# Kernel optimization log

Measured on AMD Instinct MI355X. Metric: run time of the kernel, lower is better.

Reference implementation:

```python
import jax, jax.numpy as jnp
import numpy as np

LOG_2PI = 1.8378770664093453  # log(2*pi)

B, N_FEAT = 4096, 1024
R, K, D = 64, 32, 16  # n_regions, n_batch (distributions per region), region size


def setup_inputs() -> dict:
    key = jax.random.key(0)
    k1, k2, k3, k4 = jax.random.split(key, 4)
    x = jax.random.normal(k1, (B, N_FEAT), dtype=jnp.float32)
    # Regions: partition-like index sets over the feature space (equal size D).
    regions = jax.random.randint(k2, (R, D), 0, N_FEAT, dtype=jnp.int64)
    # Per-region diag-Gaussian params (means ~ N(0, 0.1), scales near 1.0).
    means = 0.1 * jax.random.normal(k3, (R, K, D), dtype=jnp.float32)
    scales = 0.9 + 0.2 * jax.random.uniform(k4, (R, K, D), dtype=jnp.float32)
    return {"x": x, "regions": regions, "means": means, "scales": scales}


def reference(x, regions, means, scales):
    # Gather per-region features in one shot: [B, R, D]
    xg = x[:, regions]
    # Diag-Gaussian log-prob, broadcast over the K distributions per region.
    # z: [B, R, K, D]
    z = (xg[:, :, None, :] - means[None]) / scales[None]
    log_det = jnp.sum(jnp.log(scales), axis=-1)  # [R, K]
    ll = -0.5 * jnp.sum(z * z, axis=-1) - log_det[None] - 0.5 * D * LOG_2PI
    return ll  # [B, R, K] == stack over regions of MVNDiag.log_prob
```

## Files before the change

### kernel.cpp

```cpp
#include <hip/hip_runtime.h>

typedef __attribute__((ext_vector_type(8))) short short8;
typedef __attribute__((ext_vector_type(4))) float floatx4;

#define NB 4096
#define NF 1024
#define NR 64
#define NK 32
#define ND 16
#define HALF_D_LOG2PI 14.702988531274762f

__device__ __forceinline__ unsigned f2bf_bits(float f) {
    unsigned u = __float_as_uint(f);
    return (u + 0x7fffu + ((u >> 16) & 1u)) >> 16;
}
__device__ __forceinline__ float bf_bits2f(unsigned b) {
    return __uint_as_float(b << 16);
}

__global__ __launch_bounds__(256) void prep_kernel(
    const float* __restrict__ means, const float* __restrict__ scales,
    unsigned short* __restrict__ wfrag, float* __restrict__ cv)
{
    __shared__ float Asm[NK][ND];
    __shared__ float Bsm[NK][ND];
    __shared__ float csum[NK][8];
    const int r = blockIdx.x;
    const int t = threadIdx.x;

    {
        int k  = t >> 3;
        int d0 = (t & 7) * 2;
        const float* m = means  + ((size_t)r * NK + k) * ND + d0;
        const float* s = scales + ((size_t)r * NK + k) * ND + d0;
        float partial = 0.f;
#pragma unroll
        for (int q = 0; q < 2; ++q) {
            float sd = s[q], md = m[q];
            float a  = 1.f / sd;
            float a2 = a * a;
            Asm[k][d0 + q] = -0.5f * a2;
            Bsm[k][d0 + q] = md * a2;
            float c = md * a;
            partial += -0.5f * c * c - logf(sd);
        }
        csum[k][t & 7] = partial;
    }
    __syncthreads();
    if (t < NK) {
        float acc = 0.f;
#pragma unroll
        for (int q = 0; q < 8; ++q) acc += csum[t][q];
        cv[r * NK + t] = acc - HALF_D_LOG2PI;
    }

    const int ks   = t >> 7;
    const int nt   = (t >> 6) & 1;
    const int lane = t & 63;
    const int n    = lane & 15;
    const int qd   = lane >> 4;
    const int kk   = nt * 16 + n;
    unsigned px[4];
#pragma unroll
    for (int j2 = 0; j2 < 4; ++j2) {
        int j  = j2 * 2;
        int d0 = (qd * 8 + j) & 15;
        int d1 = (qd * 8 + j + 1) & 15;
        float v0 = ks ? Bsm[kk][d0] : Asm[kk][d0];
        float v1 = ks ? Bsm[kk][d1] : Asm[kk][d1];
        px[j2] = f2bf_bits(v0) | (f2bf_bits(v1) << 16);
    }
    *(uint4*)(wfrag + ((((size_t)r * 2 + ks) * 2 + nt) * 64 + lane) * 8) = *(uint4*)px;
}

__global__ __launch_bounds__(256, 2) void fused_kernel(
    const float* __restrict__ x, const int* __restrict__ regions,
    const unsigned short* __restrict__ wfrag, const float* __restrict__ cv,
    float* __restrict__ out)
{
    __shared__ __align__(16) char lds[73728];
    float* xs   = (float*)lds;
    int*   ridx = (int*)(lds + 16 * 1028 * 4);
    unsigned short* xg = (unsigned short*)lds;

    const int t  = threadIdx.x;
    const int bt = blockIdx.x;
    const int r0 = blockIdx.y * 32;
    const int b0 = bt * 16;

    for (int j = t; j < 32 * ND; j += 256) {
        int rr = j >> 4, d = j & 15;
        ridx[rr * 17 + d] = regions[(r0 + rr) * ND + d];
    }
    {
        const float4* src = (const float4*)(x + (size_t)b0 * NF);
#pragma unroll
        for (int i = 0; i < 16; ++i)
            *(float4*)(xs + i * 1028 + t * 4) = src[i * 256 + t];
    }
    __syncthreads();

    const int rl = t & 31;
    const int bA = t >> 5;
    int idxv[ND];
#pragma unroll
    for (int d = 0; d < ND; ++d) idxv[d] = ridx[rl * 17 + d];

    unsigned pk[2][32];
#pragma unroll
    for (int pp = 0; pp < 2; ++pp) {
        const int b = bA + pp * 8;
#pragma unroll
        for (int d = 0; d < ND; d += 2) {
            float x0 = xs[b * 1028 + idxv[d]];
            float x1 = xs[b * 1028 + idxv[d + 1]];
            float q0 = x0 * x0, q1 = x1 * x1;
            unsigned h20 = f2bf_bits(q0), h21 = f2bf_bits(q1);
            unsigned l20 = f2bf_bits(q0 - bf_bits2f(h20));
            unsigned l21 = f2bf_bits(q1 - bf_bits2f(h21));
            unsigned h0  = f2bf_bits(x0), h1 = f2bf_bits(x1);
            unsigned l0  = f2bf_bits(x0 - bf_bits2f(h0));
            unsigned l1  = f2bf_bits(x1 - bf_bits2f(h1));
            int di = d >> 1;
            pk[pp][di]      = h20 | (h21 << 16);
            pk[pp][8 + di]  = l20 | (l21 << 16);
            pk[pp][16 + di] = h0  | (h1 << 16);
            pk[pp][24 + di] = l0  | (l1 << 16);
        }
    }
    __syncthreads();

    {
        const int s = rl & 7;
#pragma unroll
        for (int pp = 0; pp < 2; ++pp) {
            int row = rl * 16 + bA + pp * 8;
            uint4* base = (uint4*)(xg + row * 72);
#pragma unroll
            for (int q = 0; q < 8; ++q) base[q ^ s] = ((uint4*)pk[pp])[q];
        }
    }
    __syncthreads();

    const int wv   = t >> 6;
    const int L    = t & 63;
    const int col  = L & 15;
    const int quad = L >> 4;
    const short* wfs = (const short*)wfrag;

#pragma unroll 2
    for (int i = 0; i < 8; ++i) {
        int rloc = wv * 8 + i;
        int r    = r0 + rloc;
        int row  = rloc * 16 + col;
        int s    = rloc & 7;
        const uint4* base = (const uint4*)(xg + row * 72);
        uint4 ca0 = base[quad ^ s];
        uint4 ca1 = base[(4 + quad) ^ s];
        short8 a0 = *(short8*)&ca0;
        short8 a1 = *(short8*)&ca1;

        size_t wb = ((size_t)r * 4) * 512 + (size_t)L * 8;
        short8 w00 = *(const short8*)(wfs + wb);
        short8 w01 = *(const short8*)(wfs + wb + 512);
        short8 w10 = *(const short8*)(wfs + wb + 1024);
        short8 w11 = *(const short8*)(wfs + wb + 1536);

        floatx4 acc0 = {0.f, 0.f, 0.f, 0.f};
        floatx4 acc1 = {0.f, 0.f, 0.f, 0.f};
        acc0 = __builtin_amdgcn_mfma_f32_16x16x32_bf16(a0, w00, acc0, 0, 0, 0);
        acc0 = __builtin_amdgcn_mfma_f32_16x16x32_bf16(a1, w10, acc0, 0, 0, 0);
        acc1 = __builtin_amdgcn_mfma_f32_16x16x32_bf16(a0, w01, acc1, 0, 0, 0);
        acc1 = __builtin_amdgcn_mfma_f32_16x16x32_bf16(a1, w11, acc1, 0, 0, 0);

        float c0 = cv[r * NK + col];
        float c1 = cv[r * NK + 16 + col];
        int brow = bt * 16 + quad * 4;
#pragma unroll
        for (int g = 0; g < 4; ++g) {
            size_t ob = (size_t)(brow + g) * (NR * NK) + (size_t)r * NK;
            out[ob + col]      = acc0[g] + c0;
            out[ob + 16 + col] = acc1[g] + c1;
        }
    }
}

extern "C" void kernel_launch(void* const* d_in, const int* in_sizes, int n_in,
                              void* d_out, int out_size, void* d_ws, size_t ws_size,
                              hipStream_t stream) {
    const float* x       = (const float*)d_in[0];
    const int*   regions = (const int*)d_in[1];
    const float* means   = (const float*)d_in[2];
    const float* scales  = (const float*)d_in[3];
    float* out = (float*)d_out;

    char* ws = (char*)d_ws;
    unsigned short* wfrag = (unsigned short*)ws;
    float*          cvp   = (float*)(ws + 262144);

    prep_kernel<<<dim3(NR), 256, 0, stream>>>(means, scales, wfrag, cvp);
    fused_kernel<<<dim3(NB / 16, 2), 256, 0, stream>>>(x, regions, wfrag, cvp, out);
}
```

Baseline: 85.56 us.

## Drop bf16 hi/lo split, halve MFMA K, and move to 512-thread blocks

The gathered features x and x^2 are now converted to a single bf16 each instead of a bf16 hi+lo pair, so the MFMA reduction dimension shrinks from 64 to 32. Each region/batch tile needs two MFMAs instead of four, and the weight fragments and LDS staging are halved. Blocks grow to 512 threads, one batch row per thread, with a smaller LDS footprint to allow more occupancy. The cost is lower accuracy: x^2 in plain bf16 loses precision, which may break the tolerance on the log-likelihood.

Measured after the change: 83.50 us. 2.4% less time.

```diff
diff --git a/kernel.cpp b/kernel.cpp
--- a/kernel.cpp
+++ b/kernel.cpp
@@ -13,9 +13,6 @@
 __device__ __forceinline__ unsigned f2bf_bits(float f) {
     unsigned u = __float_as_uint(f);
     return (u + 0x7fffu + ((u >> 16) & 1u)) >> 16;
-}
-__device__ __forceinline__ float bf_bits2f(unsigned b) {
-    return __uint_as_float(b << 16);
 }
 
 __global__ __launch_bounds__(256) void prep_kernel(
@@ -54,91 +51,78 @@
         cv[r * NK + t] = acc - HALF_D_LOG2PI;
     }
 
-    const int ks   = t >> 7;
-    const int nt   = (t >> 6) & 1;
-    const int lane = t & 63;
-    const int n    = lane & 15;
-    const int qd   = lane >> 4;
-    const int kk   = nt * 16 + n;
-    unsigned px[4];
+    if (t < 128) {
+        const int nt   = t >> 6;
+        const int lane = t & 63;
+        const int n    = lane & 15;
+        const int qd   = lane >> 4;
+        const int kk   = nt * 16 + n;
+        unsigned px[4];
 #pragma unroll
-    for (int j2 = 0; j2 < 4; ++j2) {
-        int j  = j2 * 2;
-        int d0 = (qd * 8 + j) & 15;
-        int d1 = (qd * 8 + j + 1) & 15;
-        float v0 = ks ? Bsm[kk][d0] : Asm[kk][d0];
-        float v1 = ks ? Bsm[kk][d1] : Asm[kk][d1];
-        px[j2] = f2bf_bits(v0) | (f2bf_bits(v1) << 16);
+        for (int j2 = 0; j2 < 4; ++j2) {
+            int K0 = qd * 8 + j2 * 2;
+            int K1 = K0 + 1;
+            float v0 = (K0 < 16) ? Asm[kk][K0] : Bsm[kk][K0 - 16];
+            float v1 = (K1 < 16) ? Asm[kk][K1] : Bsm[kk][K1 - 16];
+            px[j2] = f2bf_bits(v0) | (f2bf_bits(v1) << 16);
+        }
+        *(uint4*)(wfrag + (((size_t)r * 2 + nt) * 64 + lane) * 8) = *(uint4*)px;
     }
-    *(uint4*)(wfrag + ((((size_t)r * 2 + ks) * 2 + nt) * 64 + lane) * 8) = *(uint4*)px;
 }
 
-__global__ __launch_bounds__(256, 2) void fused_kernel(
+__global__ __launch_bounds__(512, 4) void fused_kernel(
     const float* __restrict__ x, const int* __restrict__ regions,
     const unsigned short* __restrict__ wfrag, const float* __restrict__ cv,
     float* __restrict__ out)
 {
-    __shared__ __align__(16) char lds[73728];
-    float* xs   = (float*)lds;
-    int*   ridx = (int*)(lds + 16 * 1028 * 4);
-    unsigned short* xg = (unsigned short*)lds;
+    __shared__ __align__(16) char lds[67968];
+    float*    xs   = (float*)lds;
+    int*      ridx = (int*)(lds + 16 * 1028 * 4);
+    unsigned* xgd  = (unsigned*)lds;
 
     const int t  = threadIdx.x;
     const int bt = blockIdx.x;
     const int r0 = blockIdx.y * 32;
     const int b0 = bt * 16;
 
-    for (int j = t; j < 32 * ND; j += 256) {
-        int rr = j >> 4, d = j & 15;
+    {
+        int rr = t >> 4, d = t & 15;
         ridx[rr * 17 + d] = regions[(r0 + rr) * ND + d];
     }
     {
         const float4* src = (const float4*)(x + (size_t)b0 * NF);
 #pragma unroll
-        for (int i = 0; i < 16; ++i)
-            *(float4*)(xs + i * 1028 + t * 4) = src[i * 256 + t];
+        for (int i = 0; i < 8; ++i) {
+            int j = t + i * 512;
+            int row = j >> 8, c4 = j & 255;
+            *(float4*)(xs + row * 1028 + c4 * 4) = src[row * 256 + c4];
+        }
     }
     __syncthreads();
 
     const int rl = t & 31;
-    const int bA = t >> 5;
+    const int bb = t >> 5;
     int idxv[ND];
 #pragma unroll
     for (int d = 0; d < ND; ++d) idxv[d] = ridx[rl * 17 + d];
 
-    unsigned pk[2][32];
+    unsigned pk[16];
 #pragma unroll
-    for (int pp = 0; pp < 2; ++pp) {
-        const int b = bA + pp * 8;
-#pragma unroll
-        for (int d = 0; d < ND; d += 2) {
-            float x0 = xs[b * 1028 + idxv[d]];
-            float x1 = xs[b * 1028 + idxv[d + 1]];
-            float q0 = x0 * x0, q1 = x1 * x1;
-            unsigned h20 = f2bf_bits(q0), h21 = f2bf_bits(q1);
-            unsigned l20 = f2bf_bits(q0 - bf_bits2f(h20));
-            unsigned l21 = f2bf_bits(q1 - bf_bits2f(h21));
-            unsigned h0  = f2bf_bits(x0), h1 = f2bf_bits(x1);
-            unsigned l0  = f2bf_bits(x0 - bf_bits2f(h0));
-            unsigned l1  = f2bf_bits(x1 - bf_bits2f(h1));
-            int di = d >> 1;
-            pk[pp][di]      = h20 | (h21 << 16);
-            pk[pp][8 + di]  = l20 | (l21 << 16);
-            pk[pp][16 + di] = h0  | (h1 << 16);
-            pk[pp][24 + di] = l0  | (l1 << 16);
-        }
+    for (int d = 0; d < ND; d += 2) {
+        float x0 = xs[bb * 1028 + idxv[d]];
+        float x1 = xs[bb * 1028 + idxv[d + 1]];
+        pk[d >> 1]       = f2bf_bits(x0 * x0) | (f2bf_bits(x1 * x1) << 16);
+        pk[8 + (d >> 1)] = f2bf_bits(x0)      | (f2bf_bits(x1)      << 16);
     }
     __syncthreads();
 
     {
-        const int s = rl & 7;
+        int row = rl * 16 + bb;
+        int s   = rl & 3;
+        unsigned* wp = xgd + row * 20;
 #pragma unroll
-        for (int pp = 0; pp < 2; ++pp) {
-            int row = rl * 16 + bA + pp * 8;
-            uint4* base = (uint4*)(xg + row * 72);
-#pragma unroll
-            for (int q = 0; q < 8; ++q) base[q ^ s] = ((uint4*)pk[pp])[q];
-        }
+        for (int c = 0; c < 4; ++c)
+            *(uint4*)(wp + ((c ^ s) << 2)) = ((uint4*)pk)[c];
     }
     __syncthreads();
 
@@ -148,30 +132,23 @@
     const int quad = L >> 4;
     const short* wfs = (const short*)wfrag;
 
-#pragma unroll 2
-    for (int i = 0; i < 8; ++i) {
-        int rloc = wv * 8 + i;
+#pragma unroll
+    for (int i = 0; i < 4; ++i) {
+        int rloc = wv * 4 + i;
         int r    = r0 + rloc;
         int row  = rloc * 16 + col;
-        int s    = rloc & 7;
-        const uint4* base = (const uint4*)(xg + row * 72);
-        uint4 ca0 = base[quad ^ s];
-        uint4 ca1 = base[(4 + quad) ^ s];
-        short8 a0 = *(short8*)&ca0;
-        short8 a1 = *(short8*)&ca1;
+        int s    = rloc & 3;
+        const unsigned* rp = xgd + row * 20;
+        uint4 ca = *(const uint4*)(rp + ((quad ^ s) << 2));
+        short8 a = *(short8*)&ca;
 
-        size_t wb = ((size_t)r * 4) * 512 + (size_t)L * 8;
-        short8 w00 = *(const short8*)(wfs + wb);
-        short8 w01 = *(const short8*)(wfs + wb + 512);
-        short8 w10 = *(const short8*)(wfs + wb + 1024);
-        short8 w11 = *(const short8*)(wfs + wb + 1536);
+        size_t wb = (size_t)r * 2 * 512 + (size_t)L * 8;
+        short8 w0 = *(const short8*)(wfs + wb);
+        short8 w1 = *(const short8*)(wfs + wb + 512);
 
-        floatx4 acc0 = {0.f, 0.f, 0.f, 0.f};
-        floatx4 acc1 = {0.f, 0.f, 0.f, 0.f};
-        acc0 = __builtin_amdgcn_mfma_f32_16x16x32_bf16(a0, w00, acc0, 0, 0, 0);
-        acc0 = __builtin_amdgcn_mfma_f32_16x16x32_bf16(a1, w10, acc0, 0, 0, 0);
-        acc1 = __builtin_amdgcn_mfma_f32_16x16x32_bf16(a0, w01, acc1, 0, 0, 0);
-        acc1 = __builtin_amdgcn_mfma_f32_16x16x32_bf16(a1, w11, acc1, 0, 0, 0);
+        floatx4 z = {0.f, 0.f, 0.f, 0.f};
+        floatx4 acc0 = __builtin_amdgcn_mfma_f32_16x16x32_bf16(a, w0, z, 0, 0, 0);
+        floatx4 acc1 = __builtin_amdgcn_mfma_f32_16x16x32_bf16(a, w1, z, 0, 0, 0);
 
         float c0 = cv[r * NK + col];
         float c1 = cv[r * NK + 16 + col];
@@ -196,8 +173,8 @@
 
     char* ws = (char*)d_ws;
     unsigned short* wfrag = (unsigned short*)ws;
-    float*          cvp   = (float*)(ws + 262144);
+    float*          cvp   = (float*)(ws + 131072);
 
     prep_kernel<<<dim3(NR), 256, 0, stream>>>(means, scales, wfrag, cvp);
-    fused_kernel<<<dim3(NB / 16, 2), 256, 0, stream>>>(x, regions, wfrag, cvp, out);
+    fused_kernel<<<dim3(NB / 16, 2), 512, 0, stream>>>(x, regions, wfrag, cvp, out);
 }
```
